# Kernel tuning notes

Measured on AMD Instinct MI355X. Metric: run time of the kernel, lower is better.

Reference implementation:

```python
import jax, jax.numpy as jnp
import numpy as np

EMBED_DIM = 512
NUM_HEADS = 8
HEAD_DIM = EMBED_DIM // NUM_HEADS
SCALING = HEAD_DIM ** (-0.5)
LAMBDA = 1.0
T = 128
B = 8


def setup_inputs() -> dict:
    key = jax.random.key(0)
    ks = jax.random.split(key, 8)
    d = EMBED_DIM
    # xavier-uniform-ish scale for weights
    w_lim = float(np.sqrt(6.0 / (3 * d + d)))
    o_lim = float(np.sqrt(6.0 / (d + d)))
    return {
        "query": jax.random.normal(ks[0], (T, B, d), jnp.float32),
        "key": jax.random.normal(ks[1], (T, B, d), jnp.float32),
        "value": jax.random.normal(ks[2], (T, B, d), jnp.float32),
        "correlation_bias": jax.random.normal(ks[3], (B, T, T, T), jnp.float32) * 0.1,
        "in_proj_weight": jax.random.uniform(ks[4], (3 * d, d), jnp.float32, -w_lim, w_lim),
        "in_proj_bias": jnp.zeros((3 * d,), jnp.float32),
        "out_w": jax.random.uniform(ks[5], (d, d), jnp.float32, -o_lim, o_lim),
        "out_b": jnp.zeros((d,), jnp.float32),
    }


def reference(query, key, value, correlation_bias, in_proj_weight, in_proj_bias, out_w, out_b):
    tgt_len, bsz, d = query.shape
    h, hd = NUM_HEADS, HEAD_DIM
    # split packed in-projection
    q = query @ in_proj_weight[:d].T + in_proj_bias[:d]
    k = key @ in_proj_weight[d:2 * d].T + in_proj_bias[d:2 * d]
    v = value @ in_proj_weight[2 * d:].T + in_proj_bias[2 * d:]
    q = q * SCALING
    # [T, B, D] -> [B*H, T, hd]
    q = q.reshape(tgt_len, bsz * h, hd).transpose(1, 0, 2)
    k = k.reshape(tgt_len, bsz * h, hd).transpose(1, 0, 2)
    v = v.reshape(tgt_len, bsz * h, hd).transpose(1, 0, 2)
    # trilinear score cube: [B*H, Tq, Tk, Tv]
    scores = jnp.einsum('iat,ibt,ict->iabc', q, k, v)
    # expand correlation bias over heads: [B,Tq,Tk,Tv] -> [B*H,Tq,Tk,Tv]
    bias = jnp.broadcast_to(
        correlation_bias[:, None], (bsz, h, tgt_len, tgt_len, tgt_len)
    ).reshape(bsz * h, tgt_len, tgt_len, tgt_len)
    scores = scores + LAMBDA * bias
    # mean/max fusion over Tv, softmax over Tk
    fused = jnp.mean(scores, axis=-1) + jnp.max(scores, axis=-1)
    w = jax.nn.softmax(fused.astype(jnp.float32), axis=-1).astype(fused.dtype)
    # bmm with q (note: attends over q itself, Tk == Tq required)
    attn = jnp.einsum('iab,ibd->iad', w, q)
    attn = attn.transpose(1, 0, 2).reshape(tgt_len, bsz, d)
    return attn @ out_w.T + out_b
```

## Files before the change

kernel.cpp:

```cpp
#include <hip/hip_runtime.h>
#include <math.h>

#define SCALING 0.125f

typedef __attribute__((ext_vector_type(8))) short short8;
typedef __attribute__((ext_vector_type(4))) float f32x4;

static __device__ __forceinline__ unsigned short bf16r(float x) {
  unsigned int u = __float_as_uint(x);
  u += 0x7fffu + ((u >> 16) & 1u);
  return (unsigned short)(u >> 16);
}
static __device__ __forceinline__ float bf16f(unsigned short h) {
  return __uint_as_float(((unsigned int)h) << 16);
}
static __device__ __forceinline__ unsigned int pk_bf16(float lo, float hi) {
  unsigned int ua = __float_as_uint(lo);
  unsigned int ub = __float_as_uint(hi);
  ua += 0x7fffu + ((ua >> 16) & 1u);
  ub += 0x7fffu + ((ub >> 16) & 1u);
  return __builtin_amdgcn_perm(ub, ua, 0x07060302u);
}
static __device__ __forceinline__ void split4(float4 x, ushort4& h, ushort4& l) {
  h.x = bf16r(x.x); l.x = bf16r(x.x - bf16f(h.x));
  h.y = bf16r(x.y); l.y = bf16r(x.y - bf16f(h.y));
  h.z = bf16r(x.z); l.z = bf16r(x.z - bf16f(h.z));
  h.w = bf16r(x.w); l.w = bf16r(x.w - bf16f(h.w));
}
union U4S8 { uint4 u; short8 s; };

__global__ __launch_bounds__(256)
void projmm_kernel(const float* __restrict__ query,
                   const float* __restrict__ key,
                   const float* __restrict__ value,
                   const float* __restrict__ W,
                   const float* __restrict__ bias,
                   float* __restrict__ qh, float* __restrict__ kh,
                   unsigned short* __restrict__ vh) {
  __shared__ __align__(16) unsigned short Ah[64 * 72];
  __shared__ __align__(16) unsigned short Al[64 * 72];
  __shared__ __align__(16) unsigned short Bh[64 * 72];
  __shared__ __align__(16) unsigned short Bl[64 * 72];
  const int n0 = blockIdx.x * 64;
  const int g = n0 >> 9;
  const float* __restrict__ X = (g == 0) ? query : (g == 1) ? key : value;
  const int m0 = blockIdx.y * 64;
  const int tid = threadIdx.x;
  const int w = tid >> 6, lane = tid & 63;
  const int quad = lane >> 4, n15 = lane & 15;
  const int srow = tid >> 2;
  const int scol = (tid & 3) * 16;

  f32x4 acc[4];
#pragma unroll
  for (int nt = 0; nt < 4; ++nt) acc[nt] = (f32x4){0.f, 0.f, 0.f, 0.f};

  float4 av[4], bv[4];
#pragma unroll
  for (int jj = 0; jj < 4; ++jj) {
    av[jj] = *(const float4*)&X[(m0 + srow) * 512 + scol + 4 * jj];
    bv[jj] = *(const float4*)&W[(n0 + srow) * 512 + scol + 4 * jj];
  }

  for (int k0 = 0; k0 < 512; k0 += 64) {
    __syncthreads();
#pragma unroll
    for (int jj = 0; jj < 4; ++jj) {
      ushort4 hh, ll;
      split4(av[jj], hh, ll);
      *(ushort4*)&Ah[srow * 72 + scol + 4 * jj] = hh;
      *(ushort4*)&Al[srow * 72 + scol + 4 * jj] = ll;
      split4(bv[jj], hh, ll);
      *(ushort4*)&Bh[srow * 72 + scol + 4 * jj] = hh;
      *(ushort4*)&Bl[srow * 72 + scol + 4 * jj] = ll;
    }
    __syncthreads();
    if (k0 + 64 < 512) {
#pragma unroll
      for (int jj = 0; jj < 4; ++jj) {
        av[jj] = *(const float4*)&X[(m0 + srow) * 512 + k0 + 64 + scol + 4 * jj];
        bv[jj] = *(const float4*)&W[(n0 + srow) * 512 + k0 + 64 + scol + 4 * jj];
      }
    }
#pragma unroll
    for (int kk = 0; kk < 2; ++kk) {
      short8 ah = *(const short8*)&Ah[(w * 16 + n15) * 72 + kk * 32 + quad * 8];
      short8 al = *(const short8*)&Al[(w * 16 + n15) * 72 + kk * 32 + quad * 8];
#pragma unroll
      for (int nt = 0; nt < 4; ++nt) {
        short8 bh = *(const short8*)&Bh[(nt * 16 + n15) * 72 + kk * 32 + quad * 8];
        short8 bl = *(const short8*)&Bl[(nt * 16 + n15) * 72 + kk * 32 + quad * 8];
        acc[nt] = __builtin_amdgcn_mfma_f32_16x16x32_bf16(ah, bh, acc[nt], 0, 0, 0);
        acc[nt] = __builtin_amdgcn_mfma_f32_16x16x32_bf16(ah, bl, acc[nt], 0, 0, 0);
        acc[nt] = __builtin_amdgcn_mfma_f32_16x16x32_bf16(al, bh, acc[nt], 0, 0, 0);
      }
    }
  }

#pragma unroll
  for (int nt = 0; nt < 4; ++nt) {
    const int j = n0 + nt * 16 + n15;
    const int jj = j & 511;
    const int head = jj >> 6;
    const int hd = jj & 63;
    const float bj = bias[j];
#pragma unroll
    for (int r = 0; r < 4; ++r) {
      const int row = m0 + w * 16 + quad * 4 + r;
      const int t = row >> 3;
      const int batch = row & 7;
      const int i = batch * 8 + head;
      const int idx = ((i << 7) + t) * 64 + hd;
      const float val = acc[nt][r] + bj;
      if (g == 0)      qh[idx] = val * SCALING;
      else if (g == 1) kh[idx] = val;
      else             vh[idx] = bf16r(val);
    }
  }
}

__global__ __launch_bounds__(512, 4)
void score_kernel(const float* __restrict__ qh,
                  const float* __restrict__ kh,
                  const unsigned short* __restrict__ vh,
                  const float* __restrict__ cbias,
                  float* __restrict__ attn) {
  __shared__ __align__(16) unsigned short Vs[2][128 * 72];
  __shared__ float rowS[8 * 128];

  const int ab = blockIdx.x;
  const int batch = ab >> 7;
  const int a = ab & 127;
  const int tid = threadIdx.x;
  const int w = tid >> 6;
  const int lane = tid & 63;
  const int quad = lane >> 4;
  const int n15 = lane & 15;
  const int col8 = (tid & 7) * 8;
  const int brow = w * 16 + n15;

  const float* __restrict__ bp = cbias + (size_t)ab * 16384;
  f32x4 biasReg[8];
#pragma unroll
  for (int ic = 0; ic < 8; ++ic)
    biasReg[ic] = *(const f32x4*)&bp[brow * 128 + ic * 16 + quad * 4];

  short8 bf0, bf1;
  {
    const int i = batch * 8;
    const float* __restrict__ kb = kh + (size_t)i * 8192;
    const float* __restrict__ qa = qh + ((size_t)i * 128 + a) * 64;
    f32x4 k0a = *(const f32x4*)&kb[brow * 64 + quad * 8];
    f32x4 k0b = *(const f32x4*)&kb[brow * 64 + quad * 8 + 4];
    f32x4 k1a = *(const f32x4*)&kb[brow * 64 + 32 + quad * 8];
    f32x4 k1b = *(const f32x4*)&kb[brow * 64 + 32 + quad * 8 + 4];
    f32x4 q0a = *(const f32x4*)&qa[quad * 8];
    f32x4 q0b = *(const f32x4*)&qa[quad * 8 + 4];
    f32x4 q1a = *(const f32x4*)&qa[32 + quad * 8];
    f32x4 q1b = *(const f32x4*)&qa[32 + quad * 8 + 4];
    k0a *= q0a; k0b *= q0b; k1a *= q1a; k1b *= q1b;
    U4S8 u0, u1;
    u0.u.x = pk_bf16(k0a[0], k0a[1]); u0.u.y = pk_bf16(k0a[2], k0a[3]);
    u0.u.z = pk_bf16(k0b[0], k0b[1]); u0.u.w = pk_bf16(k0b[2], k0b[3]);
    u1.u.x = pk_bf16(k1a[0], k1a[1]); u1.u.y = pk_bf16(k1a[2], k1a[3]);
    u1.u.z = pk_bf16(k1b[0], k1b[1]); u1.u.w = pk_bf16(k1b[2], k1b[3]);
    bf0 = u0.s; bf1 = u1.s;
    const uint4* __restrict__ vb4 = (const uint4*)(vh + (size_t)i * 8192);
    *(uint4*)&Vs[0][(tid >> 3) * 72 + col8] = vb4[tid];
    *(uint4*)&Vs[0][(64 + (tid >> 3)) * 72 + col8] = vb4[512 + tid];
  }
  __syncthreads();

  for (int h = 0; h < 8; ++h) {
    const int buf = h & 1;

    uint4 vreg0, vreg1;
    f32x4 kr0a, kr0b, kr1a, kr1b, qr0a, qr0b, qr1a, qr1b;
    if (h < 7) {
      const int in = batch * 8 + h + 1;
      const float* __restrict__ kb = kh + (size_t)in * 8192;
      const float* __restrict__ qa = qh + ((size_t)in * 128 + a) * 64;
      const uint4* __restrict__ vb4 = (const uint4*)(vh + (size_t)in * 8192);
      vreg0 = vb4[tid];
      vreg1 = vb4[512 + tid];
      kr0a = *(const f32x4*)&kb[brow * 64 + quad * 8];
      kr0b = *(const f32x4*)&kb[brow * 64 + quad * 8 + 4];
      kr1a = *(const f32x4*)&kb[brow * 64 + 32 + quad * 8];
      kr1b = *(const f32x4*)&kb[brow * 64 + 32 + quad * 8 + 4];
      qr0a = *(const f32x4*)&qa[quad * 8];
      qr0b = *(const f32x4*)&qa[quad * 8 + 4];
      qr1a = *(const f32x4*)&qa[32 + quad * 8];
      qr1b = *(const f32x4*)&qa[32 + quad * 8 + 4];
    }

    f32x4 acc[8];
#pragma unroll
    for (int ic = 0; ic < 8; ++ic) {
      short8 a0 = *(const short8*)&Vs[buf][(ic * 16 + n15) * 72 + quad * 8];
      short8 a1 = *(const short8*)&Vs[buf][(ic * 16 + n15) * 72 + 32 + quad * 8];
      f32x4 t = __builtin_amdgcn_mfma_f32_16x16x32_bf16(a0, bf0, biasReg[ic], 0, 0, 0);
      acc[ic] = __builtin_amdgcn_mfma_f32_16x16x32_bf16(a1, bf1, t, 0, 0, 0);
    }

    if (h < 7) {
      const int nb = buf ^ 1;
      *(uint4*)&Vs[nb][(tid >> 3) * 72 + col8] = vreg0;
      *(uint4*)&Vs[nb][(64 + (tid >> 3)) * 72 + col8] = vreg1;
      kr0a *= qr0a; kr0b *= qr0b; kr1a *= qr1a; kr1b *= qr1b;
      U4S8 u0, u1;
      u0.u.x = pk_bf16(kr0a[0], kr0a[1]); u0.u.y = pk_bf16(kr0a[2], kr0a[3]);
      u0.u.z = pk_bf16(kr0b[0], kr0b[1]); u0.u.w = pk_bf16(kr0b[2], kr0b[3]);
      u1.u.x = pk_bf16(kr1a[0], kr1a[1]); u1.u.y = pk_bf16(kr1a[2], kr1a[3]);
      u1.u.z = pk_bf16(kr1b[0], kr1b[1]); u1.u.w = pk_bf16(kr1b[2], kr1b[3]);
      bf0 = u0.s; bf1 = u1.s;
    }

    float fsum = 0.f;
    float fmx = -INFINITY;
#pragma unroll
    for (int ic = 0; ic < 8; ++ic) {
      const float v0 = acc[ic][0];
      const float v1 = acc[ic][1];
      const float v2 = acc[ic][2];
      const float v3 = acc[ic][3];
      fsum += (v0 + v1) + (v2 + v3);
      fmx = fmaxf(fmx, fmaxf(fmaxf(v0, v1), fmaxf(v2, v3)));
    }
    fsum += __shfl_xor(fsum, 16, 64);
    fmx = fmaxf(fmx, __shfl_xor(fmx, 16, 64));
    fsum += __shfl_xor(fsum, 32, 64);
    fmx = fmaxf(fmx, __shfl_xor(fmx, 32, 64));
    if (quad == 0) rowS[h * 128 + w * 16 + n15] = fsum * (1.0f / 128.0f) + fmx;

    __syncthreads();
  }

  {
    const int h = w;
    const int i = batch * 8 + h;
    float f0 = rowS[h * 128 + lane], f1 = rowS[h * 128 + 64 + lane];
    float m = fmaxf(f0, f1);
#pragma unroll
    for (int off = 32; off >= 1; off >>= 1) m = fmaxf(m, __shfl_xor(m, off, 64));
    const float e0 = expf(f0 - m), e1 = expf(f1 - m);
    float s = e0 + e1;
#pragma unroll
    for (int off = 32; off >= 1; off >>= 1) s += __shfl_xor(s, off, 64);
    const float inv = 1.0f / s;
    rowS[h * 128 + lane] = e0 * inv;
    rowS[h * 128 + 64 + lane] = e1 * inv;
    const float* __restrict__ qp = qh + (size_t)i * 8192 + lane;
    float acc2 = 0.0f;
#pragma unroll 8
    for (int b = 0; b < 128; ++b)
      acc2 = fmaf(rowS[h * 128 + b], qp[b * 64], acc2);
    attn[((size_t)a * 8 + batch) * 512 + h * 64 + lane] = acc2;
  }
}

__global__ __launch_bounds__(256)
void outmm_kernel(const float* __restrict__ Xa,
                  const float* __restrict__ W,
                  const float* __restrict__ bias,
                  float* __restrict__ out) {
  __shared__ __align__(16) unsigned short Ah[64 * 72];
  __shared__ __align__(16) unsigned short Al[64 * 72];
  __shared__ __align__(16) unsigned short Bh[32 * 72];
  __shared__ __align__(16) unsigned short Bl[32 * 72];
  const int n0 = blockIdx.x * 32;
  const int m0 = blockIdx.y * 64;
  const int tid = threadIdx.x;
  const int w = tid >> 6, lane = tid & 63;
  const int quad = lane >> 4, n15 = lane & 15;
  const int srow = tid >> 2;
  const int scol = (tid & 3) * 16;
  const bool doB = tid >= 128;
  const int brow = (tid & 127) >> 2;
  const int bcol = (tid & 3) * 16;

  f32x4 acc[2];
#pragma unroll
  for (int nt = 0; nt < 2; ++nt) acc[nt] = (f32x4){0.f, 0.f, 0.f, 0.f};

  float4 av[4], bv[4];
#pragma unroll
  for (int jj = 0; jj < 4; ++jj)
    av[jj] = *(const float4*)&Xa[(m0 + srow) * 512 + scol + 4 * jj];
  if (doB) {
#pragma unroll
    for (int jj = 0; jj < 4; ++jj)
      bv[jj] = *(const float4*)&W[(n0 + brow) * 512 + bcol + 4 * jj];
  }

  for (int k0 = 0; k0 < 512; k0 += 64) {
    __syncthreads();
#pragma unroll
    for (int jj = 0; jj < 4; ++jj) {
      ushort4 hh, ll;
      split4(av[jj], hh, ll);
      *(ushort4*)&Ah[srow * 72 + scol + 4 * jj] = hh;
      *(ushort4*)&Al[srow * 72 + scol + 4 * jj] = ll;
    }
    if (doB) {
#pragma unroll
      for (int jj = 0; jj < 4; ++jj) {
        ushort4 hh, ll;
        split4(bv[jj], hh, ll);
        *(ushort4*)&Bh[brow * 72 + bcol + 4 * jj] = hh;
        *(ushort4*)&Bl[brow * 72 + bcol + 4 * jj] = ll;
      }
    }
    __syncthreads();
    if (k0 + 64 < 512) {
#pragma unroll
      for (int jj = 0; jj < 4; ++jj)
        av[jj] = *(const float4*)&Xa[(m0 + srow) * 512 + k0 + 64 + scol + 4 * jj];
      if (doB) {
#pragma unroll
        for (int jj = 0; jj < 4; ++jj)
          bv[jj] = *(const float4*)&W[(n0 + brow) * 512 + k0 + 64 + bcol + 4 * jj];
      }
    }
#pragma unroll
    for (int kk = 0; kk < 2; ++kk) {
      short8 ah = *(const short8*)&Ah[(w * 16 + n15) * 72 + kk * 32 + quad * 8];
      short8 al = *(const short8*)&Al[(w * 16 + n15) * 72 + kk * 32 + quad * 8];
#pragma unroll
      for (int nt = 0; nt < 2; ++nt) {
        short8 bh = *(const short8*)&Bh[(nt * 16 + n15) * 72 + kk * 32 + quad * 8];
        short8 bl = *(const short8*)&Bl[(nt * 16 + n15) * 72 + kk * 32 + quad * 8];
        acc[nt] = __builtin_amdgcn_mfma_f32_16x16x32_bf16(ah, bh, acc[nt], 0, 0, 0);
        acc[nt] = __builtin_amdgcn_mfma_f32_16x16x32_bf16(ah, bl, acc[nt], 0, 0, 0);
        acc[nt] = __builtin_amdgcn_mfma_f32_16x16x32_bf16(al, bh, acc[nt], 0, 0, 0);
      }
    }
  }

#pragma unroll
  for (int nt = 0; nt < 2; ++nt) {
    const int j = n0 + nt * 16 + n15;
    const float bj = bias[j];
#pragma unroll
    for (int r = 0; r < 4; ++r) {
      const int row = m0 + w * 16 + quad * 4 + r;
      out[(size_t)row * 512 + j] = acc[nt][r] + bj;
    }
  }
}

extern "C" void kernel_launch(void* const* d_in, const int* in_sizes, int n_in,
                              void* d_out, int out_size, void* d_ws,
                              size_t ws_size, hipStream_t stream) {
  const float* query = (const float*)d_in[0];
  const float* key   = (const float*)d_in[1];
  const float* value = (const float*)d_in[2];
  const float* cbias = (const float*)d_in[3];
  const float* W     = (const float*)d_in[4];
  const float* pb    = (const float*)d_in[5];
  const float* out_w = (const float*)d_in[6];
  const float* out_b = (const float*)d_in[7];
  float* out = (float*)d_out;

  float* ws = (float*)d_ws;
  float* qh = ws;
  float* kh = ws + 524288;
  unsigned short* vh = (unsigned short*)(ws + 1048576);
  float* attn = ws + 1048576 + 262144;

  projmm_kernel<<<dim3(24, 16), 256, 0, stream>>>(query, key, value, W, pb,
                                                  qh, kh, vh);
  score_kernel<<<1024, 512, 0, stream>>>(qh, kh, vh, cbias, attn);
  outmm_kernel<<<dim3(16, 16), 256, 0, stream>>>(attn, out_w, out_b, out);
}
```

Before: 194.2 us.

## Stage V for four heads at once to cut per-head block barriers

The V tiles for four heads are now loaded into shared memory together, in a buffer four times larger, instead of double-buffering one head at a time. The next four heads are prefetched into registers during head 2 and written to shared memory at head 3. This replaces eight per-head __syncthreads with roughly three barriers in total, and the head loop is fully unrolled. In exchange, shared memory grows from about 40KB to about 78KB and 8 uint4 prefetch registers are held, which may reduce occupancy below the launch-bounds target of 4 blocks per CU.

```diff
diff --git a/kernel.cpp b/kernel.cpp
--- a/kernel.cpp
+++ b/kernel.cpp
@@ -125,7 +125,7 @@
                   const unsigned short* __restrict__ vh,
                   const float* __restrict__ cbias,
                   float* __restrict__ attn) {
-  __shared__ __align__(16) unsigned short Vs[2][128 * 72];
+  __shared__ __align__(16) unsigned short Vs[4 * 128 * 72];
   __shared__ float rowS[8 * 128];
 
   const int ab = blockIdx.x;
@@ -136,7 +136,6 @@
   const int lane = tid & 63;
   const int quad = lane >> 4;
   const int n15 = lane & 15;
-  const int col8 = (tid & 7) * 8;
   const int brow = w * 16 + n15;
 
   const float* __restrict__ bp = cbias + (size_t)ab * 16384;
@@ -147,9 +146,17 @@
 
   short8 bf0, bf1;
   {
-    const int i = batch * 8;
-    const float* __restrict__ kb = kh + (size_t)i * 8192;
-    const float* __restrict__ qa = qh + ((size_t)i * 128 + a) * 64;
+    const int i0 = batch * 8;
+    const uint4* __restrict__ vb4 = (const uint4*)(vh + (size_t)i0 * 8192);
+#pragma unroll
+    for (int j = 0; j < 8; ++j) {
+      const int gidx = j * 512 + tid;
+      const int head = gidx >> 10;
+      const int uidx = gidx & 1023;
+      *(uint4*)&Vs[head * 9216 + (uidx >> 3) * 72 + (uidx & 7) * 8] = vb4[gidx];
+    }
+    const float* __restrict__ kb = kh + (size_t)i0 * 8192;
+    const float* __restrict__ qa = qh + ((size_t)i0 * 128 + a) * 64;
     f32x4 k0a = *(const f32x4*)&kb[brow * 64 + quad * 8];
     f32x4 k0b = *(const f32x4*)&kb[brow * 64 + quad * 8 + 4];
     f32x4 k1a = *(const f32x4*)&kb[brow * 64 + 32 + quad * 8];
@@ -165,24 +172,19 @@
     u1.u.x = pk_bf16(k1a[0], k1a[1]); u1.u.y = pk_bf16(k1a[2], k1a[3]);
     u1.u.z = pk_bf16(k1b[0], k1b[1]); u1.u.w = pk_bf16(k1b[2], k1b[3]);
     bf0 = u0.s; bf1 = u1.s;
-    const uint4* __restrict__ vb4 = (const uint4*)(vh + (size_t)i * 8192);
-    *(uint4*)&Vs[0][(tid >> 3) * 72 + col8] = vb4[tid];
-    *(uint4*)&Vs[0][(64 + (tid >> 3)) * 72 + col8] = vb4[512 + tid];
   }
   __syncthreads();
 
+  uint4 vpref[8];
+#pragma unroll
   for (int h = 0; h < 8; ++h) {
-    const int buf = h & 1;
-
-    uint4 vreg0, vreg1;
+    const int i = batch * 8 + h;
+
     f32x4 kr0a, kr0b, kr1a, kr1b, qr0a, qr0b, qr1a, qr1b;
     if (h < 7) {
-      const int in = batch * 8 + h + 1;
+      const int in = i + 1;
       const float* __restrict__ kb = kh + (size_t)in * 8192;
       const float* __restrict__ qa = qh + ((size_t)in * 128 + a) * 64;
-      const uint4* __restrict__ vb4 = (const uint4*)(vh + (size_t)in * 8192);
-      vreg0 = vb4[tid];
-      vreg1 = vb4[512 + tid];
       kr0a = *(const f32x4*)&kb[brow * 64 + quad * 8];
       kr0b = *(const f32x4*)&kb[brow * 64 + quad * 8 + 4];
       kr1a = *(const f32x4*)&kb[brow * 64 + 32 + quad * 8];
@@ -192,20 +194,55 @@
       qr1a = *(const f32x4*)&qa[32 + quad * 8];
       qr1b = *(const f32x4*)&qa[32 + quad * 8 + 4];
     }
-
+    if (h == 2) {
+      const uint4* __restrict__ vb4 =
+          (const uint4*)(vh + ((size_t)batch * 8 + 4) * 8192);
+#pragma unroll
+      for (int j = 0; j < 8; ++j) vpref[j] = vb4[j * 512 + tid];
+    }
+
+    const unsigned short* __restrict__ Vb = &Vs[(h & 3) * 9216];
     f32x4 acc[8];
 #pragma unroll
     for (int ic = 0; ic < 8; ++ic) {
-      short8 a0 = *(const short8*)&Vs[buf][(ic * 16 + n15) * 72 + quad * 8];
-      short8 a1 = *(const short8*)&Vs[buf][(ic * 16 + n15) * 72 + 32 + quad * 8];
+      short8 a0 = *(const short8*)&Vb[(ic * 16 + n15) * 72 + quad * 8];
+      short8 a1 = *(const short8*)&Vb[(ic * 16 + n15) * 72 + 32 + quad * 8];
       f32x4 t = __builtin_amdgcn_mfma_f32_16x16x32_bf16(a0, bf0, biasReg[ic], 0, 0, 0);
       acc[ic] = __builtin_amdgcn_mfma_f32_16x16x32_bf16(a1, bf1, t, 0, 0, 0);
     }
 
+    float fsum = 0.f;
+    float fmx = -INFINITY;
+#pragma unroll
+    for (int ic = 0; ic < 8; ++ic) {
+      const float v0 = acc[ic][0];
+      const float v1 = acc[ic][1];
+      const float v2 = acc[ic][2];
+      const float v3 = acc[ic][3];
+      const float s01 = v0 + v1, s23 = v2 + v3;
+      fsum += s01 + s23;
+      const float m01 = fmaxf(v0, v1), m23 = fmaxf(v2, v3);
+      fmx = fmaxf(fmaxf(m01, m23), fmx);
+    }
+    fsum += __shfl_xor(fsum, 16, 64);
+    fmx = fmaxf(fmx, __shfl_xor(fmx, 16, 64));
+    fsum += __shfl_xor(fsum, 32, 64);
+    fmx = fmaxf(fmx, __shfl_xor(fmx, 32, 64));
+    if (quad == 0) rowS[h * 128 + w * 16 + n15] = fsum * (1.0f / 128.0f) + fmx;
+
+    if (h == 3) {
+      __syncthreads();
+#pragma unroll
+      for (int j = 0; j < 8; ++j) {
+        const int gidx = j * 512 + tid;
+        const int head = gidx >> 10;
+        const int uidx = gidx & 1023;
+        *(uint4*)&Vs[head * 9216 + (uidx >> 3) * 72 + (uidx & 7) * 8] = vpref[j];
+      }
+      __syncthreads();
+    }
+
     if (h < 7) {
-      const int nb = buf ^ 1;
-      *(uint4*)&Vs[nb][(tid >> 3) * 72 + col8] = vreg0;
-      *(uint4*)&Vs[nb][(64 + (tid >> 3)) * 72 + col8] = vreg1;
       kr0a *= qr0a; kr0b *= qr0b; kr1a *= qr1a; kr1b *= qr1b;
       U4S8 u0, u1;
       u0.u.x = pk_bf16(kr0a[0], kr0a[1]); u0.u.y = pk_bf16(kr0a[2], kr0a[3]);
@@ -214,26 +251,8 @@
       u1.u.z = pk_bf16(kr1b[0], kr1b[1]); u1.u.w = pk_bf16(kr1b[2], kr1b[3]);
       bf0 = u0.s; bf1 = u1.s;
     }
-
-    float fsum = 0.f;
-    float fmx = -INFINITY;
-#pragma unroll
-    for (int ic = 0; ic < 8; ++ic) {
-      const float v0 = acc[ic][0];
-      const float v1 = acc[ic][1];
-      const float v2 = acc[ic][2];
-      const float v3 = acc[ic][3];
-      fsum += (v0 + v1) + (v2 + v3);
-      fmx = fmaxf(fmx, fmaxf(fmaxf(v0, v1), fmaxf(v2, v3)));
-    }
-    fsum += __shfl_xor(fsum, 16, 64);
-    fmx = fmaxf(fmx, __shfl_xor(fmx, 16, 64));
-    fsum += __shfl_xor(fsum, 32, 64);
-    fmx = fmaxf(fmx, __shfl_xor(fmx, 32, 64));
-    if (quad == 0) rowS[h * 128 + w * 16 + n15] = fsum * (1.0f / 128.0f) + fmx;
-
-    __syncthreads();
-  }
+  }
+  __syncthreads();
 
   {
     const int h = w;
```

Result: slower. 212.3 us (+9.3%).
